# Performance work log

Hardware: AMD Instinct MI355X
Metric: run time of the kernel (lower is better)

Reference implementation:

```python
import jax, jax.numpy as jnp
import numpy as np

N_EMBED = 2048
N_HEAD = 2
HEAD_SIZE = N_EMBED // N_HEAD  # 1024; mask constraint requires T <= HEAD_SIZE


def setup_inputs() -> dict:
    key = jax.random.key(0)
    ks = jax.random.split(key, 9)
    B, T, C, H, D = 32, 1024, N_EMBED, N_HEAD, HEAD_SIZE
    s = 1.0 / np.sqrt(C)
    x = jax.random.normal(ks[0], (B, T, C), dtype=jnp.float32)
    # torch Linear convention: weight (out_features, in_features), y = x @ W.T + b
    Wq = jax.random.normal(ks[1], (H, D, C), dtype=jnp.float32) * s
    Wk = jax.random.normal(ks[2], (H, D, C), dtype=jnp.float32) * s
    Wv = jax.random.normal(ks[3], (H, D, C), dtype=jnp.float32) * s
    bq = jax.random.normal(ks[4], (H, D), dtype=jnp.float32) * 0.01
    bk = jax.random.normal(ks[5], (H, D), dtype=jnp.float32) * 0.01
    bv = jax.random.normal(ks[6], (H, D), dtype=jnp.float32) * 0.01
    Wo = jax.random.normal(ks[7], (C, H * D), dtype=jnp.float32) * s  # no bias
    return {"x": x, "Wq": Wq, "bq": bq, "Wk": Wk, "bk": bk, "Wv": Wv, "bv": bv, "Wo": Wo}


def reference(x, Wq, bq, Wk, bk, Wv, bv, Wo):
    B, T, C = x.shape
    # per-head projections, batched over heads: (B,T,C) x (H,D,C) -> (B,H,T,D)
    q = jnp.einsum('btc,hdc->bhtd', x, Wq) + bq[None, :, None, :]
    k = jnp.einsum('btc,hdc->bhtd', x, Wk) + bk[None, :, None, :]
    v = jnp.einsum('btc,hdc->bhtd', x, Wv) + bv[None, :, None, :]
    # NOTE: original scales by x.shape[-1]**-0.5 == n_embed**-0.5 (not head_size)
    scale = jnp.asarray(C, x.dtype) ** -0.5
    wei = jnp.einsum('bhtd,bhsd->bhts', q, k) * scale  # (B,H,T,T)
    causal = jnp.tril(jnp.ones((T, T), dtype=bool))
    wei = jnp.where(causal[None, None], wei, -jnp.inf)
    wei = jax.nn.softmax(wei, axis=-1)
    out = jnp.einsum('bhts,bhsd->bhtd', wei, v)  # (B,H,T,D)
    # concat heads along last dim: (B,T,H*D)
    out = out.transpose(0, 2, 1, 3).reshape(B, T, -1)
    return out @ Wo.T  # (B,T,C)
```

## Files before the change

kernel.cpp:

```cpp
#include <hip/hip_runtime.h>
#include <hip/hip_bf16.h>
#include <stdint.h>

typedef __bf16 bf16_t;
typedef __bf16 bf16x8 __attribute__((ext_vector_type(8)));
typedef float f32x4 __attribute__((ext_vector_type(4)));

#define AS1(p) ((const __attribute__((address_space(1))) void*)(uintptr_t)(p))
#define AS3(p) ((__attribute__((address_space(3))) void*)(uintptr_t)(p))

__device__ __forceinline__ void gload16(const bf16_t* g, bf16_t* l) {
  __builtin_amdgcn_global_load_lds(AS1(g), AS3(l), 16, 0, 0);
}

#define SB()      __builtin_amdgcn_sched_barrier(0);
#define BARR()    { __builtin_amdgcn_s_barrier(); __builtin_amdgcn_sched_barrier(0); }
#define VMCNT(n)  { asm volatile("s_waitcnt vmcnt(" #n ")" ::: "memory"); __builtin_amdgcn_sched_barrier(0); }
#define LGKM(n)   { asm volatile("s_waitcnt lgkmcnt(" #n ")" ::: "memory"); __builtin_amdgcn_sched_barrier(0); }

__device__ __forceinline__ void gemm256(const bf16_t* __restrict__ A, int lda,
                                        const bf16_t* __restrict__ B, int ldb,
                                        int nt, f32x4 acc[4][4], bf16_t* lds) {
  const int t = (int)threadIdx.x;
  const int lane = t & 63, wv = t >> 6;
  const int wr = wv >> 2, wc = wv & 3;
  const int fr = lane & 15, fq = lane >> 4;
  char* ldsb = (char*)lds;

  const int s0 = (t * 16) ^ (((t >> 3) & 7) << 4);
  const int r0 = s0 >> 6, q0 = (s0 >> 4) & 3;
  const bf16_t* gA = A + (size_t)r0 * lda + q0 * 8;
  const bf16_t* gB = B + (size_t)r0 * ldb + q0 * 8;

  const int swz = (fr * 64 + fq * 16) ^ (((fr >> 1) & 7) << 4);
  const int abase = wr * 4096 + swz;
  const int bbase = 32768 + wc * 4096 + swz;

  bf16x8 bb[4], aaA[2], aaB[2];

#define STAGE_A(cb, kh, kof) { \
    gload16(gA + (kof) + (kh) * 32, lds + (cb) * 32768 + (kh) * 8192 + t * 8); \
  } SB()
#define STAGE_B(cb, kh, kof) { \
    gload16(gB + (kof) + (kh) * 32, lds + (cb) * 32768 + 16384 + (kh) * 8192 + t * 8); \
  } SB()
#define READ_B(cb, kh) { \
    const char* _b = ldsb + (cb) * 65536 + (kh) * 16384 + bbase; \
    _Pragma("unroll") for (int n = 0; n < 4; ++n) bb[n] = *(const bf16x8*)(_b + n * 1024); }
#define READ_A2(cb, kh, qh, dst) { \
    const char* _a = ldsb + (cb) * 65536 + (kh) * 16384 + abase + (qh) * 2048; \
    dst[0] = *(const bf16x8*)(_a); \
    dst[1] = *(const bf16x8*)(_a + 1024); }
#define MFMA8(dst, qh) { \
    __builtin_amdgcn_s_setprio(1); \
    _Pragma("unroll") for (int qi = 0; qi < 2; ++qi) \
      _Pragma("unroll") for (int n = 0; n < 4; ++n) \
        acc[(qh) * 2 + qi][n] = __builtin_amdgcn_mfma_f32_16x16x32_bf16(dst[qi], bb[n], acc[(qh) * 2 + qi][n], 0, 0, 0); \
    __builtin_amdgcn_s_setprio(0); }

  STAGE_A(0, 0, 0) STAGE_B(0, 0, 0) STAGE_A(0, 1, 0) STAGE_B(0, 1, 0)

  int kof = 64;
  for (int tt = 0; tt < nt - 1; ++tt, kof += 64) {
    const int cb = tt & 1;
    VMCNT(2) BARR()
    READ_B(cb, 0) READ_A2(cb, 0, 0, aaA)
    STAGE_A(cb ^ 1, 0, kof)
    READ_A2(cb, 0, 1, aaB)
    STAGE_B(cb ^ 1, 0, kof)
    LGKM(2) MFMA8(aaA, 0)
    LGKM(0) MFMA8(aaB, 1)
    VMCNT(2) BARR()
    READ_B(cb, 1) READ_A2(cb, 1, 0, aaA)
    STAGE_A(cb ^ 1, 1, kof)
    READ_A2(cb, 1, 1, aaB)
    STAGE_B(cb ^ 1, 1, kof)
    LGKM(2) MFMA8(aaA, 0)
    LGKM(0) MFMA8(aaB, 1)
  }
  {
    const int cb = (nt - 1) & 1;
    VMCNT(2) BARR()
    READ_B(cb, 0) READ_A2(cb, 0, 0, aaA) READ_A2(cb, 0, 1, aaB)
    LGKM(2) MFMA8(aaA, 0)
    LGKM(0) MFMA8(aaB, 1)
    VMCNT(0) BARR()
    READ_B(cb, 1) READ_A2(cb, 1, 0, aaA) READ_A2(cb, 1, 1, aaB)
    LGKM(2) MFMA8(aaA, 0)
    LGKM(0) MFMA8(aaB, 1)
  }
#undef STAGE_A
#undef STAGE_B
#undef READ_B
#undef READ_A2
#undef MFMA8
}

#define EPI_VARS \
  const int t = (int)threadIdx.x; \
  const int lane = t & 63, w = t >> 6; \
  const int wr = w >> 2, wc = w & 3; \
  const int fr = lane & 15, fq = lane >> 4;

#define ZERO4x4(acc) \
  _Pragma("unroll") for (int _i = 0; _i < 4; ++_i) \
  _Pragma("unroll") for (int _j = 0; _j < 4; ++_j) { f32x4 _z = {0.f,0.f,0.f,0.f}; acc[_i][_j] = _z; }

__global__ void k_cvt(const float* __restrict__ s, bf16_t* __restrict__ d, long n8) {
  long i = (long)blockIdx.x * blockDim.x + threadIdx.x;
  long st = (long)gridDim.x * blockDim.x;
  for (; i < n8; i += st) {
    const float4* sp = (const float4*)(s + i * 8);
    float4 a = sp[0], b = sp[1];
    bf16x8 v;
    v[0] = (__bf16)a.x; v[1] = (__bf16)a.y; v[2] = (__bf16)a.z; v[3] = (__bf16)a.w;
    v[4] = (__bf16)b.x; v[5] = (__bf16)b.y; v[6] = (__bf16)b.z; v[7] = (__bf16)b.w;
    *(bf16x8*)(d + i * 8) = v;
  }
}

__global__ void k_cvtw(const float* __restrict__ Wq, const float* __restrict__ Wk,
                       const float* __restrict__ Wv, const float* __restrict__ Wo,
                       bf16_t* __restrict__ d) {
  long i = (long)blockIdx.x * blockDim.x + threadIdx.x;
  long st = (long)gridDim.x * blockDim.x;
  for (; i < 2097152L; i += st) {
    int r = (int)(i >> 19);
    const float* s = (r == 0 ? Wq : r == 1 ? Wk : r == 2 ? Wv : Wo) + (i & 524287L) * 8;
    float4 a = ((const float4*)s)[0], b = ((const float4*)s)[1];
    bf16x8 v;
    v[0] = (__bf16)a.x; v[1] = (__bf16)a.y; v[2] = (__bf16)a.z; v[3] = (__bf16)a.w;
    v[4] = (__bf16)b.x; v[5] = (__bf16)b.y; v[6] = (__bf16)b.z; v[7] = (__bf16)b.w;
    *(bf16x8*)(d + i * 8) = v;
  }
}

__global__ void k_fill(float* o, float v, long n) {
  long i = (long)blockIdx.x * blockDim.x + threadIdx.x;
  long st = (long)gridDim.x * blockDim.x;
  for (; i < n; i += st) o[i] = v;
}

__global__ __launch_bounds__(1024, 1) void k_qkv256(
    const bf16_t* __restrict__ xb, const bf16_t* __restrict__ Wb,
    const float* __restrict__ bq, const float* __restrict__ bk, const float* __restrict__ bv,
    bf16_t* __restrict__ Q, bf16_t* __restrict__ K, bf16_t* __restrict__ Vt) {
  __shared__ __align__(16) bf16_t lds[65536];
  int bid = (int)blockIdx.x;
  int id = (bid & 7) * 384 + (bid >> 3);
  EPI_VARS
  f32x4 acc[4][4];
  ZERO4x4(acc)

  bool vmode = id >= 2048;
  int mt = 0, ntile = 0, tok = 0, wm = 0;
  const bf16_t *Ap, *Bp;
  if (!vmode) {
    mt = id & 127; ntile = id >> 7;
    Ap = xb + (size_t)mt * 256 * 2048;
    Bp = Wb + (size_t)ntile * 256 * 2048;
  } else {
    int vb = id - 2048;
    tok = vb & 127; wm = vb >> 7;
    Ap = Wb + (size_t)(16 + wm) * 256 * 2048;
    Bp = xb + (size_t)tok * 256 * 2048;
  }
  gemm256(Ap, 2048, Bp, 2048, 32, acc, lds);

  if (!vmode) {
    int sel = ntile >> 3;
    const float* bias = sel ? bk : bq;
    bf16_t* dst = sel ? K : Q;
    int cbase = (ntile & 7) * 256 + wc * 64;
#pragma unroll
    for (int cn = 0; cn < 4; ++cn) {
      int c2 = cbase + cn * 16 + fr;
      int h = c2 >> 10, d = c2 & 1023;
      float bb = bias[c2];
#pragma unroll
      for (int qm = 0; qm < 4; ++qm) {
        f32x4 a = acc[qm][cn];
#pragma unroll
        for (int r = 0; r < 4; ++r) {
          int m = mt * 256 + wr * 64 + qm * 16 + fq * 4 + r;
          int b = m >> 10, tk = m & 1023;
          dst[(((size_t)(b * 2 + h) << 10) + tk) * 1024 + d] = (bf16_t)(a[r] + bb);
        }
      }
    }
  } else {
#pragma unroll
    for (int qm = 0; qm < 4; ++qm) {
#pragma unroll
      for (int r = 0; r < 4; ++r) {
        int gd = wm * 256 + wr * 64 + qm * 16 + fq * 4 + r;
        int h = gd >> 10, dd = gd & 1023;
        float bb = bv[gd];
#pragma unroll
        for (int cn = 0; cn < 4; ++cn) {
          int m = tok * 256 + wc * 64 + cn * 16 + fr;
          int b = m >> 10, tk = m & 1023;
          Vt[(((size_t)(b * 2 + h) << 10) + dd) * 1024 + tk] = (bf16_t)(acc[qm][cn][r] + bb);
        }
      }
    }
  }
}

__global__ __launch_bounds__(1024, 1) void k_s256(const bf16_t* __restrict__ Q,
                                                  const bf16_t* __restrict__ K,
                                                  bf16_t* __restrict__ S, int pbase) {
  __shared__ __align__(16) bf16_t lds[65536];
  int id = (int)blockIdx.x;
  int pc = id / 10, rem = id % 10;
  int ti = 0;
  while (rem > ti) { rem -= ti + 1; ++ti; }
  int tj = rem;
  size_t p = (size_t)(pbase + pc);
  EPI_VARS
  f32x4 acc[4][4];
  ZERO4x4(acc)
  gemm256(Q + (p << 20) + (size_t)ti * 256 * 1024, 1024,
          K + (p << 20) + (size_t)tj * 256 * 1024, 1024, 16, acc, lds);
  bf16_t* Sp = S + ((size_t)pc << 20);
  const float scale = 0.022097086912079608f;
#pragma unroll
  for (int qm = 0; qm < 4; ++qm)
#pragma unroll
    for (int cn = 0; cn < 4; ++cn) {
      int col = tj * 256 + wc * 64 + cn * 16 + fr;
      f32x4 a = acc[qm][cn];
#pragma unroll
      for (int r = 0; r < 4; ++r) {
        int row = ti * 256 + wr * 64 + qm * 16 + fq * 4 + r;
        Sp[((size_t)row << 10) + col] = (bf16_t)(a[r] * scale);
      }
    }
}

__global__ __launch_bounds__(256) void k_softmax(const bf16_t* __restrict__ S,
                                                 bf16_t* __restrict__ P) {
  int gw = (int)blockIdx.x * 4 + ((int)threadIdx.x >> 6);
  int pc = gw >> 10, row = gw & 1023;
  int lane = (int)threadIdx.x & 63;
  const bf16_t* s = S + ((size_t)pc << 20) + ((size_t)row << 10);
  bf16_t* p = P + ((size_t)pc << 20) + ((size_t)row << 10);
  int cend = ((row >> 8) + 1) << 8;
  bf16x8 v0 = *(const bf16x8*)(s + lane * 8);
  bf16x8 v1 = *(const bf16x8*)(s + 512 + lane * 8);
  float x[16];
  float mx = -1e30f;
#pragma unroll
  for (int j = 0; j < 8; ++j) {
    int c0 = lane * 8 + j, c1 = 512 + lane * 8 + j;
    x[j]     = (c0 <= row) ? (float)v0[j] : -1e30f;
    x[8 + j] = (c1 <= row) ? (float)v1[j] : -1e30f;
    mx = fmaxf(mx, fmaxf(x[j], x[8 + j]));
  }
  for (int o = 32; o > 0; o >>= 1) mx = fmaxf(mx, __shfl_xor(mx, o));
  float sum = 0.f;
#pragma unroll
  for (int j = 0; j < 16; ++j) {
    x[j] = (x[j] > -1e29f) ? __expf(x[j] - mx) : 0.f;
    sum += x[j];
  }
  for (int o = 32; o > 0; o >>= 1) sum += __shfl_xor(sum, o);
  float inv = 1.f / sum;
  bf16x8 o0, o1;
#pragma unroll
  for (int j = 0; j < 8; ++j) {
    o0[j] = (bf16_t)(x[j] * inv);
    o1[j] = (bf16_t)(x[8 + j] * inv);
  }
  if (lane * 8 < cend)       *(bf16x8*)(p + lane * 8) = o0;
  if (512 + lane * 8 < cend) *(bf16x8*)(p + 512 + lane * 8) = o1;
}

__global__ __launch_bounds__(1024, 1) void k_pv256(const bf16_t* __restrict__ P,
                                                   const bf16_t* __restrict__ Vt,
                                                   bf16_t* __restrict__ O, int pbase) {
  __shared__ __align__(16) bf16_t lds[65536];
  int id = (int)blockIdx.x;
  int pc = id >> 4, rem = id & 15;
  int ti = rem >> 2, dj = rem & 3;
  size_t p = (size_t)(pbase + pc);
  EPI_VARS
  f32x4 acc[4][4];
  ZERO4x4(acc)
  gemm256(P + ((size_t)pc << 20) + (size_t)ti * 256 * 1024, 1024,
          Vt + (p << 20) + (size_t)dj * 256 * 1024, 1024, (ti + 1) * 4, acc, lds);
  int b = (int)(p >> 1), h = (int)(p & 1);
#pragma unroll
  for (int qm = 0; qm < 4; ++qm)
#pragma unroll
    for (int cn = 0; cn < 4; ++cn) {
      int dcol = dj * 256 + wc * 64 + cn * 16 + fr;
      f32x4 a = acc[qm][cn];
#pragma unroll
      for (int r = 0; r < 4; ++r) {
        int tk = ti * 256 + wr * 64 + qm * 16 + fq * 4 + r;
        O[(((size_t)b << 10) + tk) * 2048 + (h << 10) + dcol] = (bf16_t)a[r];
      }
    }
}

__global__ __launch_bounds__(1024, 1) void k_out256(const bf16_t* __restrict__ O,
                                                    const bf16_t* __restrict__ W,
                                                    float* __restrict__ out) {
  __shared__ __align__(16) bf16_t lds[65536];
  int bid = (int)blockIdx.x;
  int id = (bid & 7) * 128 + (bid >> 3);
  int mt = id & 127, ntile = id >> 7;
  EPI_VARS
  f32x4 acc[4][4];
  ZERO4x4(acc)
  gemm256(O + (size_t)mt * 256 * 2048, 2048, W + (size_t)ntile * 256 * 2048, 2048, 32, acc, lds);
#pragma unroll
  for (int qm = 0; qm < 4; ++qm)
#pragma unroll
    for (int cn = 0; cn < 4; ++cn) {
      int col = ntile * 256 + wc * 64 + cn * 16 + fr;
      f32x4 a = acc[qm][cn];
#pragma unroll
      for (int r = 0; r < 4; ++r) {
        int row = mt * 256 + wr * 64 + qm * 16 + fq * 4 + r;
        out[(size_t)row * 2048 + col] = a[r];
      }
    }
}

extern "C" void kernel_launch(void* const* d_in, const int* in_sizes, int n_in,
                              void* d_out, int out_size, void* d_ws, size_t ws_size,
                              hipStream_t stream) {
  const float* x  = (const float*)d_in[0];
  const float* Wq = (const float*)d_in[1];
  const float* bq = (const float*)d_in[2];
  const float* Wk = (const float*)d_in[3];
  const float* bk = (const float*)d_in[4];
  const float* Wv = (const float*)d_in[5];
  const float* bv = (const float*)d_in[6];
  const float* Wo = (const float*)d_in[7];
  float* out = (float*)d_out;

  const size_t MiB = 1ull << 20;
  char* w = (char*)d_ws;
  bf16_t* xb    = (bf16_t*)w;
  bf16_t* Ob    = xb;
  bf16_t* Qb    = (bf16_t*)(w + 128 * MiB);
  bf16_t* Kb    = (bf16_t*)(w + 256 * MiB);
  bf16_t* Vt    = (bf16_t*)(w + 384 * MiB);
  bf16_t* Wqkvb = (bf16_t*)(w + 512 * MiB);
  bf16_t* Wob   = (bf16_t*)(w + 536 * MiB);
  bf16_t* Sc    = (bf16_t*)(w + 544 * MiB);

  size_t rem = ws_size > 544 * MiB ? ws_size - 544 * MiB : 0;
  int NP = (int)(rem / (2 * MiB));
  if (NP > 64) NP = 64;
  if (NP < 1) {
    k_fill<<<2048, 256, 0, stream>>>(out, (float)(ws_size >> 20), (long)out_size);
    return;
  }

  k_cvt<<<2048, 256, 0, stream>>>(x, xb, 8388608L);
  k_cvtw<<<2048, 256, 0, stream>>>(Wq, Wk, Wv, Wo, Wqkvb);

  k_qkv256<<<3072, 1024, 0, stream>>>(xb, Wqkvb, bq, bk, bv, Qb, Kb, Vt);

  for (int base = 0; base < 64; base += NP) {
    int np = (64 - base) < NP ? (64 - base) : NP;
    k_s256<<<np * 10, 1024, 0, stream>>>(Qb, Kb, Sc, base);
    k_softmax<<<np * 256, 256, 0, stream>>>(Sc, Sc);
    k_pv256<<<np * 16, 1024, 0, stream>>>(Sc, Vt, Ob, base);
  }

  k_out256<<<1024, 1024, 0, stream>>>(Ob, Wob, out);
}
```

Before: 1.476 ms.

## Fuse softmax into QK and PV kernels via atomic row max/sum merge

Removes the separate softmax pass. The QK^T kernel now computes per-tile row max and exp-sum and merges them into a per-row (max, sum) pair with a 64-bit atomicCAS. The PV kernel reads the raw scores, applies exp and normalization with the causal mask while staging A into LDS, then runs the MFMA loop with a 32-wide K step. This saves one full read and write of the score matrix per pair, at the cost of CAS contention, an extra init kernel, and register-path A staging in place of direct global-to-LDS loads.

Result: slower. 1.628 ms (+10.3%).

```diff
diff --git a/kernel.cpp b/kernel.cpp
--- a/kernel.cpp
+++ b/kernel.cpp
@@ -106,6 +106,19 @@
   _Pragma("unroll") for (int _i = 0; _i < 4; ++_i) \
   _Pragma("unroll") for (int _j = 0; _j < 4; ++_j) { f32x4 _z = {0.f,0.f,0.f,0.f}; acc[_i][_j] = _z; }
 
+__device__ __forceinline__ void ml_merge(unsigned long long* p, float m2, float l2) {
+  unsigned long long old = *p, assumed;
+  do {
+    assumed = old;
+    float m1 = __uint_as_float((unsigned)(assumed >> 32));
+    float l1 = __uint_as_float((unsigned)assumed);
+    float m = fmaxf(m1, m2);
+    float l = l1 * __expf(m1 - m) + l2 * __expf(m2 - m);
+    unsigned long long nv = ((unsigned long long)__float_as_uint(m) << 32) | __float_as_uint(l);
+    old = atomicCAS(p, assumed, nv);
+  } while (old != assumed);
+}
+
 __global__ void k_cvt(const float* __restrict__ s, bf16_t* __restrict__ d, long n8) {
   long i = (long)blockIdx.x * blockDim.x + threadIdx.x;
   long st = (long)gridDim.x * blockDim.x;
@@ -135,6 +148,11 @@
   }
 }
 
+__global__ void k_mlinit(unsigned long long* ml, int n) {
+  int i = (int)blockIdx.x * blockDim.x + threadIdx.x;
+  if (i < n) ml[i] = ((unsigned long long)__float_as_uint(-1e30f) << 32);
+}
+
 __global__ void k_fill(float* o, float v, long n) {
   long i = (long)blockIdx.x * blockDim.x + threadIdx.x;
   long st = (long)gridDim.x * blockDim.x;
@@ -209,7 +227,9 @@
 
 __global__ __launch_bounds__(1024, 1) void k_s256(const bf16_t* __restrict__ Q,
                                                   const bf16_t* __restrict__ K,
-                                                  bf16_t* __restrict__ S, int pbase) {
+                                                  bf16_t* __restrict__ S,
+                                                  unsigned long long* __restrict__ ML,
+                                                  int pbase) {
   __shared__ __align__(16) bf16_t lds[65536];
   int id = (int)blockIdx.x;
   int pc = id / 10, rem = id % 10;
@@ -236,59 +256,123 @@
         Sp[((size_t)row << 10) + col] = (bf16_t)(a[r] * scale);
       }
     }
-}
-
-__global__ __launch_bounds__(256) void k_softmax(const bf16_t* __restrict__ S,
-                                                 bf16_t* __restrict__ P) {
-  int gw = (int)blockIdx.x * 4 + ((int)threadIdx.x >> 6);
-  int pc = gw >> 10, row = gw & 1023;
-  int lane = (int)threadIdx.x & 63;
-  const bf16_t* s = S + ((size_t)pc << 20) + ((size_t)row << 10);
-  bf16_t* p = P + ((size_t)pc << 20) + ((size_t)row << 10);
-  int cend = ((row >> 8) + 1) << 8;
-  bf16x8 v0 = *(const bf16x8*)(s + lane * 8);
-  bf16x8 v1 = *(const bf16x8*)(s + 512 + lane * 8);
-  float x[16];
-  float mx = -1e30f;
-#pragma unroll
-  for (int j = 0; j < 8; ++j) {
-    int c0 = lane * 8 + j, c1 = 512 + lane * 8 + j;
-    x[j]     = (c0 <= row) ? (float)v0[j] : -1e30f;
-    x[8 + j] = (c1 <= row) ? (float)v1[j] : -1e30f;
-    mx = fmaxf(mx, fmaxf(x[j], x[8 + j]));
-  }
-  for (int o = 32; o > 0; o >>= 1) mx = fmaxf(mx, __shfl_xor(mx, o));
-  float sum = 0.f;
-#pragma unroll
-  for (int j = 0; j < 16; ++j) {
-    x[j] = (x[j] > -1e29f) ? __expf(x[j] - mx) : 0.f;
-    sum += x[j];
-  }
-  for (int o = 32; o > 0; o >>= 1) sum += __shfl_xor(sum, o);
-  float inv = 1.f / sum;
-  bf16x8 o0, o1;
-#pragma unroll
-  for (int j = 0; j < 8; ++j) {
-    o0[j] = (bf16_t)(x[j] * inv);
-    o1[j] = (bf16_t)(x[8 + j] * inv);
-  }
-  if (lane * 8 < cend)       *(bf16x8*)(p + lane * 8) = o0;
-  if (512 + lane * 8 < cend) *(bf16x8*)(p + 512 + lane * 8) = o1;
-}
-
-__global__ __launch_bounds__(1024, 1) void k_pv256(const bf16_t* __restrict__ P,
-                                                   const bf16_t* __restrict__ Vt,
-                                                   bf16_t* __restrict__ O, int pbase) {
-  __shared__ __align__(16) bf16_t lds[65536];
+#pragma unroll
+  for (int qm = 0; qm < 4; ++qm)
+#pragma unroll
+    for (int r = 0; r < 4; ++r) {
+      int row_gl = ti * 256 + wr * 64 + qm * 16 + fq * 4 + r;
+      float vv[4];
+      float mx = -1e30f;
+#pragma unroll
+      for (int cn = 0; cn < 4; ++cn) {
+        int col = tj * 256 + wc * 64 + cn * 16 + fr;
+        float v = acc[qm][cn][r] * scale;
+        vv[cn] = (col <= row_gl) ? v : -1e30f;
+        mx = fmaxf(mx, vv[cn]);
+      }
+#pragma unroll
+      for (int xm = 1; xm < 16; xm <<= 1) mx = fmaxf(mx, __shfl_xor(mx, xm));
+      float sm = 0.f;
+#pragma unroll
+      for (int cn = 0; cn < 4; ++cn) sm += (vv[cn] > -1e29f) ? __expf(vv[cn] - mx) : 0.f;
+#pragma unroll
+      for (int xm = 1; xm < 16; xm <<= 1) sm += __shfl_xor(sm, xm);
+      if (fr == 0 && mx > -1e29f) ml_merge(&ML[pc * 1024 + row_gl], mx, sm);
+    }
+}
+
+__global__ __launch_bounds__(1024, 1) void k_pvsm(const bf16_t* __restrict__ S,
+                                                  const bf16_t* __restrict__ Vt,
+                                                  const unsigned long long* __restrict__ ML,
+                                                  bf16_t* __restrict__ O, int pbase) {
+  __shared__ __align__(16) bf16_t lds[32768];
   int id = (int)blockIdx.x;
   int pc = id >> 4, rem = id & 15;
   int ti = rem >> 2, dj = rem & 3;
   size_t p = (size_t)(pbase + pc);
   EPI_VARS
+  char* ldsb = (char*)lds;
   f32x4 acc[4][4];
   ZERO4x4(acc)
-  gemm256(P + ((size_t)pc << 20) + (size_t)ti * 256 * 1024, 1024,
-          Vt + (p << 20) + (size_t)dj * 256 * 1024, 1024, (ti + 1) * 4, acc, lds);
+
+  const int r0l = t >> 2, kq = t & 3;
+  const int row_g = ti * 256 + r0l;
+  const bf16_t* gS = S + ((size_t)pc << 20) + ((size_t)row_g << 10) + kq * 8;
+  unsigned long long mlv = ML[pc * 1024 + row_g];
+  const float mrow = __uint_as_float((unsigned)(mlv >> 32));
+  const float lrinv = 1.0f / __uint_as_float((unsigned)mlv);
+  const int owz = (t * 16) ^ (((t >> 3) & 7) << 4);
+
+  const int s0 = (t * 16) ^ (((t >> 3) & 7) << 4);
+  const int r0 = s0 >> 6, q0 = (s0 >> 4) & 3;
+  const bf16_t* gB = Vt + (p << 20) + (size_t)dj * 256 * 1024 + (size_t)r0 * 1024 + q0 * 8;
+
+  const int swz = (fr * 64 + fq * 16) ^ (((fr >> 1) & 7) << 4);
+  const int abase = wr * 4096 + swz;
+  const int bbase = 16384 + wc * 4096 + swz;
+
+  bf16x8 bb[4], aaA[2], aaB[2], ar;
+
+#define PLOADA(kof) { ar = *(const bf16x8*)(gS + (kof)); } SB()
+#define PSTOREA(sl, kof) { \
+    bf16x8 pv8; \
+    _Pragma("unroll") for (int j = 0; j < 8; ++j) { \
+      float sv = (float)ar[j]; \
+      float pvv = __expf(sv - mrow) * lrinv; \
+      pv8[j] = ((kof) + kq * 8 + j <= row_g) ? (bf16_t)pvv : (bf16_t)0.f; \
+    } \
+    *(bf16x8*)(ldsb + (sl) * 32768 + owz) = pv8; \
+  } SB()
+#define PSTAGE_B(sl, kof) { \
+    gload16(gB + (kof), lds + (sl) * 16384 + 8192 + t * 8); \
+  } SB()
+#define PREAD_B(sl) { \
+    const char* _b = ldsb + (sl) * 32768 + bbase; \
+    _Pragma("unroll") for (int n = 0; n < 4; ++n) bb[n] = *(const bf16x8*)(_b + n * 1024); }
+#define PREAD_A2(sl, qh, dst) { \
+    const char* _a = ldsb + (sl) * 32768 + abase + (qh) * 2048; \
+    dst[0] = *(const bf16x8*)(_a); \
+    dst[1] = *(const bf16x8*)(_a + 1024); }
+#define PMFMA8(dst, qh) { \
+    __builtin_amdgcn_s_setprio(1); \
+    _Pragma("unroll") for (int qi = 0; qi < 2; ++qi) \
+      _Pragma("unroll") for (int n = 0; n < 4; ++n) \
+        acc[(qh) * 2 + qi][n] = __builtin_amdgcn_mfma_f32_16x16x32_bf16(dst[qi], bb[n], acc[(qh) * 2 + qi][n], 0, 0, 0); \
+    __builtin_amdgcn_s_setprio(0); }
+
+  const int H = (ti + 1) * 8;
+  PLOADA(0)
+  VMCNT(0)
+  PSTOREA(0, 0)
+  PSTAGE_B(0, 0)
+  LGKM(0)
+  int kof = 32;
+  for (int ww = 0; ww < H - 1; ++ww, kof += 32) {
+    const int sl = ww & 1;
+    VMCNT(0) BARR()
+    PLOADA(kof)
+    PSTAGE_B(sl ^ 1, kof)
+    PREAD_B(sl) PREAD_A2(sl, 0, aaA)
+    VMCNT(1) SB()
+    PSTOREA(sl ^ 1, kof)
+    PREAD_A2(sl, 1, aaB)
+    LGKM(3) PMFMA8(aaA, 0)
+    LGKM(0) PMFMA8(aaB, 1)
+  }
+  {
+    const int sl = (H - 1) & 1;
+    VMCNT(0) BARR()
+    PREAD_B(sl) PREAD_A2(sl, 0, aaA) PREAD_A2(sl, 1, aaB)
+    LGKM(2) PMFMA8(aaA, 0)
+    LGKM(0) PMFMA8(aaB, 1)
+  }
+#undef PLOADA
+#undef PSTOREA
+#undef PSTAGE_B
+#undef PREAD_B
+#undef PREAD_A2
+#undef PMFMA8
+
   int b = (int)(p >> 1), h = (int)(p & 1);
 #pragma unroll
   for (int qm = 0; qm < 4; ++qm)
@@ -354,12 +438,13 @@
   bf16_t* Sc    = (bf16_t*)(w + 544 * MiB);
 
   size_t rem = ws_size > 544 * MiB ? ws_size - 544 * MiB : 0;
-  int NP = (int)(rem / (2 * MiB));
+  int NP = (int)(rem / (2 * MiB + 8192));
   if (NP > 64) NP = 64;
   if (NP < 1) {
     k_fill<<<2048, 256, 0, stream>>>(out, (float)(ws_size >> 20), (long)out_size);
     return;
   }
+  unsigned long long* ML = (unsigned long long*)(w + 544 * MiB + (size_t)NP * 2 * MiB);
 
   k_cvt<<<2048, 256, 0, stream>>>(x, xb, 8388608L);
   k_cvtw<<<2048, 256, 0, stream>>>(Wq, Wk, Wv, Wo, Wqkvb);
@@ -368,9 +453,9 @@
 
   for (int base = 0; base < 64; base += NP) {
     int np = (64 - base) < NP ? (64 - base) : NP;
-    k_s256<<<np * 10, 1024, 0, stream>>>(Qb, Kb, Sc, base);
-    k_softmax<<<np * 256, 256, 0, stream>>>(Sc, Sc);
-    k_pv256<<<np * 16, 1024, 0, stream>>>(Sc, Vt, Ob, base);
+    k_mlinit<<<(np * 1024 + 255) / 256, 256, 0, stream>>>(ML, np * 1024);
+    k_s256<<<np * 10, 1024, 0, stream>>>(Qb, Kb, Sc, ML, base);
+    k_pvsm<<<np * 16, 1024, 0, stream>>>(Sc, Vt, ML, Ob, base);
   }
 
   k_out256<<<1024, 1024, 0, stream>>>(Ob, Wob, out);
```
